# Kernel tuning notes

Hardware: AMD Instinct MI355X
Metric: run time of the kernel (lower is better)

Reference implementation:

```python
import jax, jax.numpy as jnp
import numpy as np

DIM = 1024
NUM_HEADS = 16
HEAD_DIM = DIM // NUM_HEADS


def setup_inputs() -> dict:
    key = jax.random.key(0)
    ks = jax.random.split(key, 9)
    s = 1.0 / np.sqrt(DIM)
    x = jax.random.normal(ks[0], (2, 2048, DIM), dtype=jnp.float32)
    Wq = jax.random.normal(ks[1], (DIM, DIM), dtype=jnp.float32) * s
    bq = jax.random.normal(ks[2], (DIM,), dtype=jnp.float32) * s
    Wk = jax.random.normal(ks[3], (DIM, DIM), dtype=jnp.float32) * s
    bk = jax.random.normal(ks[4], (DIM,), dtype=jnp.float32) * s
    Wv = jax.random.normal(ks[5], (DIM, DIM), dtype=jnp.float32) * s
    bv = jax.random.normal(ks[6], (DIM,), dtype=jnp.float32) * s
    Wo = jax.random.normal(ks[7], (DIM, DIM), dtype=jnp.float32) * s
    bo = jax.random.normal(ks[8], (DIM,), dtype=jnp.float32) * s
    return {"x": x, "Wq": Wq, "bq": bq, "Wk": Wk, "bk": bk,
            "Wv": Wv, "bv": bv, "Wo": Wo, "bo": bo}


def _softmax_one(x, axis=-1):
    # softmax with +1 in the denominator (quiet attention)
    x = x - jnp.max(x, axis=axis, keepdims=True)
    ex = jnp.exp(x)
    return ex / (1.0 + jnp.sum(ex, axis=axis, keepdims=True))


def reference(x, Wq, bq, Wk, bk, Wv, bv, Wo, bo):
    B, L, D = x.shape
    H, hd = NUM_HEADS, HEAD_DIM
    q = (x @ Wq + bq).reshape(B, L, H, hd).transpose(0, 2, 1, 3)  # b h l d
    k = (x @ Wk + bk).reshape(B, L, H, hd).transpose(0, 2, 1, 3)
    v = (x @ Wv + bv).reshape(B, L, H, hd).transpose(0, 2, 1, 3)
    scores = jnp.einsum('bhqd,bhkd->bhqk', q, k) / np.sqrt(hd).astype(np.float32)
    # causal additive mask: -inf above the diagonal (matches torch generate_square_subsequent_mask)
    causal = jnp.triu(jnp.full((L, L), -jnp.inf, dtype=scores.dtype), k=1)
    scores = scores + causal
    attn = _softmax_one(scores, axis=-1)
    ctx = jnp.einsum('bhqk,bhkd->bhqd', attn, v)
    ctx = ctx.transpose(0, 2, 1, 3).reshape(B, L, D)
    return ctx @ Wo + bo
```

## Files before the change

kernel.cpp:

```cpp
#include <hip/hip_runtime.h>
#include <hip/hip_bf16.h>
#include <cstdint>
#include <cstddef>

#define DIMN 1024
#define NHEAD 16
#define HDIM 64
#define NB 2
#define SEQ 2048
#define MROWS 4096
#define BHN 32
#define QKV_STRIDE 4194304
#define BH_ELEMS 131072

typedef float f32x4 __attribute__((ext_vector_type(4)));
typedef __bf16 bf16x8 __attribute__((ext_vector_type(8)));

__device__ __forceinline__ void async_copy16(const void* g, void* l) {
    __builtin_amdgcn_global_load_lds(
        (__attribute__((address_space(1))) void*)(g),
        (__attribute__((address_space(3))) void*)(l), 16, 0, 0);
}

__device__ __forceinline__ unsigned short bf16_bits(float f) {
    __hip_bfloat16 hb = __float2bfloat16(f);
    return *(unsigned short*)&hb;
}

__global__ __launch_bounds__(256) void prep_kernel(
        const float* __restrict__ x, const float* __restrict__ bq,
        const float* __restrict__ bk, const float* __restrict__ bv,
        const float* __restrict__ Wq, const float* __restrict__ Wk,
        const float* __restrict__ Wv, const float* __restrict__ Wo,
        __hip_bfloat16* __restrict__ xbf, float* __restrict__ biasq,
        __hip_bfloat16* __restrict__ wqkvt, __hip_bfloat16* __restrict__ wot) {
    __shared__ float tile[32][33];
    const int bid = blockIdx.x;
    const int t = threadIdx.x;
    if (bid < 4096) {
        int i = (bid * 256 + t) * 4;
        float4 v = *(const float4*)(x + i);
        xbf[i + 0] = __float2bfloat16(v.x);
        xbf[i + 1] = __float2bfloat16(v.y);
        xbf[i + 2] = __float2bfloat16(v.z);
        xbf[i + 3] = __float2bfloat16(v.w);
    } else if (bid < 4099) {
        int base = (bid - 4096) * 1024 + t * 4;
#pragma unroll
        for (int e = 0; e < 4; e++) {
            int gi = base + e;
            int which = gi >> 10, off = gi & 1023;
            float v = (which == 0) ? bq[off] : (which == 1) ? bk[off] : bv[off];
            biasq[gi] = v;
        }
    } else {
        int rr = bid - 4099;
        int z = rr >> 10;
        int tid = rr & 1023;
        int n0 = (tid & 31) * 32, k0 = (tid >> 5) * 32;
        const float* in = (z == 0) ? Wq : (z == 1) ? Wk : (z == 2) ? Wv : Wo;
        __hip_bfloat16* out = (z == 3) ? wot : wqkvt + (size_t)z * DIMN * DIMN;
        int tx = t & 31, ty = t >> 5;
#pragma unroll
        for (int r = 0; r < 32; r += 8)
            tile[ty + r][tx] = in[(size_t)(k0 + ty + r) * DIMN + n0 + tx];
        __syncthreads();
#pragma unroll
        for (int r = 0; r < 32; r += 8)
            out[(size_t)(n0 + ty + r) * DIMN + k0 + tx] =
                __float2bfloat16(tile[tx][ty + r]);
    }
}

__global__ __launch_bounds__(256) void gemm_qkv_kernel(
        const __hip_bfloat16* __restrict__ A, const __hip_bfloat16* __restrict__ Bt,
        const float* __restrict__ bias, __hip_bfloat16* __restrict__ qkv,
        __hip_bfloat16* __restrict__ vt) {
    __shared__ __align__(16) unsigned short As[128 * 32];
    __shared__ __align__(16) unsigned short Bs[128 * 32];
    const int t = threadIdx.x;
    const int m0 = blockIdx.y * 128;
    const int n0 = blockIdx.x * 128;
    const int lane = t & 63;
    const int w = t >> 6;
    const int wm = (w >> 1) * 64;
    const int wn = (w & 1) * 64;
    const int r16 = lane & 15;
    const int quad = lane >> 4;

    f32x4 acc[4][4];
#pragma unroll
    for (int i = 0; i < 4; i++)
#pragma unroll
        for (int j = 0; j < 4; j++) acc[i][j] = (f32x4){0.f, 0.f, 0.f, 0.f};

    const int rowA = t >> 2;
    const int kch = (t & 3) * 8;

    for (int k0 = 0; k0 < DIMN; k0 += 32) {
        __syncthreads();
#pragma unroll
        for (int r = 0; r < 2; r++) {
            int row = rowA + r * 64;
            async_copy16(A + (size_t)(m0 + row) * DIMN + k0 + kch,
                         (char*)As + (size_t)(row * 4 + (t & 3)) * 16);
            async_copy16(Bt + (size_t)(n0 + row) * DIMN + k0 + kch,
                         (char*)Bs + (size_t)(row * 4 + (t & 3)) * 16);
        }
        __syncthreads();

        bf16x8 af[4], bfr[4];
#pragma unroll
        for (int i = 0; i < 4; i++)
            af[i] = *(const bf16x8*)&As[(wm + i * 16 + r16) * 32 + quad * 8];
#pragma unroll
        for (int j = 0; j < 4; j++)
            bfr[j] = *(const bf16x8*)&Bs[(wn + j * 16 + r16) * 32 + quad * 8];
#pragma unroll
        for (int i = 0; i < 4; i++)
#pragma unroll
            for (int j = 0; j < 4; j++)
                acc[i][j] = __builtin_amdgcn_mfma_f32_16x16x32_bf16(
                    af[i], bfr[j], acc[i][j], 0, 0, 0);
    }

#pragma unroll
    for (int i = 0; i < 4; i++)
#pragma unroll
        for (int j = 0; j < 4; j++) {
            int n = n0 + wn + j * 16 + r16;
            float bv = bias[n];
            int which = n >> 10, rem = n & 1023;
            int h = rem >> 6, d = rem & 63;
            int mbase = m0 + wm + i * 16 + quad * 4;
            int b = mbase >> 11;
            int lrow = mbase & 2047;
            int bh = b * NHEAD + h;
            if (which == 2) {
                ushort4 pk;
                pk.x = bf16_bits(acc[i][j][0] + bv);
                pk.y = bf16_bits(acc[i][j][1] + bv);
                pk.z = bf16_bits(acc[i][j][2] + bv);
                pk.w = bf16_bits(acc[i][j][3] + bv);
                *(ushort4*)(vt + (size_t)bh * BH_ELEMS + (size_t)d * SEQ + lrow) = pk;
            } else {
#pragma unroll
                for (int r = 0; r < 4; r++) {
                    float v = acc[i][j][r] + bv;
                    if (which == 0) v *= 0.125f;
                    qkv[(size_t)which * QKV_STRIDE + (size_t)bh * BH_ELEMS +
                        (size_t)(lrow + r) * 64 + d] = __float2bfloat16(v);
                }
            }
        }
}

__global__ __launch_bounds__(256) void gemm_out_kernel(
        const __hip_bfloat16* __restrict__ A, const __hip_bfloat16* __restrict__ Bt,
        const float* __restrict__ bias, float* __restrict__ outp) {
    __shared__ __align__(16) unsigned short As[64 * 32];
    __shared__ __align__(16) unsigned short Bs[128 * 32];
    const int t = threadIdx.x;
    const int m0 = blockIdx.y * 64;
    const int n0 = blockIdx.x * 128;
    const int lane = t & 63;
    const int w = t >> 6;
    const int wm = (w >> 1) * 32;
    const int wn = (w & 1) * 64;
    const int r16 = lane & 15;
    const int quad = lane >> 4;

    f32x4 acc[2][4];
#pragma unroll
    for (int i = 0; i < 2; i++)
#pragma unroll
        for (int j = 0; j < 4; j++) acc[i][j] = (f32x4){0.f, 0.f, 0.f, 0.f};

    const int rowA = t >> 2;
    const int kch = (t & 3) * 8;

    for (int k0 = 0; k0 < DIMN; k0 += 32) {
        __syncthreads();
        async_copy16(A + (size_t)(m0 + rowA) * DIMN + k0 + kch, (char*)As + t * 16);
#pragma unroll
        for (int r = 0; r < 2; r++) {
            int row = rowA + r * 64;
            async_copy16(Bt + (size_t)(n0 + row) * DIMN + k0 + kch,
                         (char*)Bs + (size_t)(row * 4 + (t & 3)) * 16);
        }
        __syncthreads();

        bf16x8 af[2], bfr[4];
#pragma unroll
        for (int i = 0; i < 2; i++)
            af[i] = *(const bf16x8*)&As[(wm + i * 16 + r16) * 32 + quad * 8];
#pragma unroll
        for (int j = 0; j < 4; j++)
            bfr[j] = *(const bf16x8*)&Bs[(wn + j * 16 + r16) * 32 + quad * 8];
#pragma unroll
        for (int i = 0; i < 2; i++)
#pragma unroll
            for (int j = 0; j < 4; j++)
                acc[i][j] = __builtin_amdgcn_mfma_f32_16x16x32_bf16(
                    af[i], bfr[j], acc[i][j], 0, 0, 0);
    }

#pragma unroll
    for (int i = 0; i < 2; i++)
#pragma unroll
        for (int j = 0; j < 4; j++) {
            int n = n0 + wn + j * 16 + r16;
            float bv = bias[n];
#pragma unroll
            for (int r = 0; r < 4; r++) {
                int m = m0 + wm + i * 16 + quad * 4 + r;
                outp[(size_t)m * DIMN + n] = acc[i][j][r] + bv;
            }
        }
}

__global__ __launch_bounds__(512, 4) void attn_mfma_kernel(
        const __hip_bfloat16* __restrict__ qkv, const __hip_bfloat16* __restrict__ vt,
        __hip_bfloat16* __restrict__ ctxout) {
    __shared__ __align__(16) unsigned short SMEM[28672];

    const int bx = blockIdx.x;
    const int g = bx >> 5;
    const int qt = (g < 8) ? 15 - g : g - 8;
    const int bh = bx & 31;
    const int t = threadIdx.x;
    const int lane = t & 63;
    const int w = t >> 6;
    const int half = w >> 2;
    const int wq = w & 3;
    const int r16 = lane & 15;
    const int quad = lane >> 4;
    const int qbase = qt * 128 + wq * 32;
    const int swz = quad ^ ((r16 >> 1) & 3);
    const int pkey = (r16 >> 1) & 3;

    const __hip_bfloat16* Qg = qkv + (size_t)bh * BH_ELEMS;
    const __hip_bfloat16* Kg = qkv + (size_t)QKV_STRIDE + (size_t)bh * BH_ELEMS;
    const __hip_bfloat16* Vtg = vt + (size_t)bh * BH_ELEMS;

    unsigned short* PsW = SMEM + 24576 + w * 512;

    const int cb_kp = (t & 511) >> 8;
    const int cb_rr = ((t & 511) >> 2) & 63;
    const int cb_cg = ((t & 511) & 3) ^ ((cb_rr >> 1) & 3);

    bf16x8 bq[2][2];
#pragma unroll
    for (int ng = 0; ng < 2; ng++)
#pragma unroll
        for (int kp = 0; kp < 2; kp++)
            bq[ng][kp] = *(const bf16x8*)(Qg + (size_t)(qbase + ng * 16 + r16) * 64 +
                                          kp * 32 + quad * 8);

    f32x4 oT[4][2];
#pragma unroll
    for (int mt = 0; mt < 4; mt++)
#pragma unroll
        for (int ng = 0; ng < 2; ng++) oT[mt][ng] = (f32x4){0.f, 0.f, 0.f, 0.f};
    float m_run[2] = {-1e30f, -1e30f};
    float z_run[2] = {0.f, 0.f};

    const int niter = qt + 1;

#pragma unroll
    for (int it = 0; it < 2; it++) {
        int cl = it * 512 + t;
        int ktile = (cl >> 9) ? (qt + 1) : 0;
        async_copy16(Kg + (size_t)(ktile * 64 + cb_rr) * 64 + cb_kp * 32 + cb_cg * 8,
                     (char*)SMEM + (size_t)cl * 16);
    }

#pragma unroll 1
    for (int i = 0; i < niter; i++) {
        const int curb = i & 1;
        __syncthreads();

#pragma unroll
        for (int it = 0; it < 2; it++) {
            int cl = it * 512 + t;
            int ktile = (cl >> 9) ? (qt + 1 + i) : i;
            async_copy16(Vtg + (size_t)cb_rr * SEQ + ktile * 64 + cb_kp * 32 + cb_cg * 8,
                         (char*)SMEM + 32768 + (size_t)cl * 16);
        }
        if (i + 1 < niter) {
            int ktA = i + 1;
            int ktB = qt + 2 + i; if (ktB > 31) ktB = 31;
#pragma unroll
            for (int it = 0; it < 2; it++) {
                int cl = it * 512 + t;
                int ktile = (cl >> 9) ? ktB : ktA;
                async_copy16(Kg + (size_t)(ktile * 64 + cb_rr) * 64 + cb_kp * 32 + cb_cg * 8,
                             (char*)SMEM + (size_t)(curb ^ 1) * 16384 + (size_t)cl * 16);
            }
        }

        const int ktile = half ? (qt + 1 + i) : i;
        const bool active = (ktile * 64 <= qbase + 31);

        f32x4 st[4][2];
        if (active) {
            const unsigned short* KsW = SMEM + curb * 8192 + half * 4096;
#pragma unroll
            for (int mt = 0; mt < 4; mt++)
#pragma unroll
                for (int ng = 0; ng < 2; ng++) st[mt][ng] = (f32x4){0.f, 0.f, 0.f, 0.f};
#pragma unroll
            for (int mt = 0; mt < 4; mt++)
#pragma unroll
                for (int kp = 0; kp < 2; kp++) {
                    bf16x8 ak = *(const bf16x8*)&KsW[kp * 2048 + (mt * 16 + r16) * 32 + swz * 8];
                    st[mt][0] = __builtin_amdgcn_mfma_f32_16x16x32_bf16(ak, bq[0][kp], st[mt][0], 0, 0, 0);
                    st[mt][1] = __builtin_amdgcn_mfma_f32_16x16x32_bf16(ak, bq[1][kp], st[mt][1], 0, 0, 0);
                }

            if (ktile * 64 + 63 > qbase) {
#pragma unroll
                for (int mt = 0; mt < 4; mt++) {
                    int kb = ktile * 64 + mt * 16 + quad * 4;
#pragma unroll
                    for (int ng = 0; ng < 2; ng++) {
                        int q = qbase + ng * 16 + r16;
#pragma unroll
                        for (int r = 0; r < 4; r++)
                            if (kb + r > q) st[mt][ng][r] = -__builtin_inff();
                    }
                }
            }

#pragma unroll
            for (int mt = 0; mt < 4; mt++)
#pragma unroll
                for (int ng = 0; ng < 2; ng++) {
                    float s0 = st[mt][ng][0], s1 = st[mt][ng][1];
                    float s2 = st[mt][ng][2], s3 = st[mt][ng][3];
                    m_run[ng] = fmaxf(m_run[ng], fmaxf(fmaxf(s0, s1), fmaxf(s2, s3)));
                    float p0 = __expf(s0), p1 = __expf(s1);
                    float p2 = __expf(s2), p3 = __expf(s3);
                    z_run[ng] += (p0 + p1) + (p2 + p3);
                    st[mt][ng][0] = p0; st[mt][ng][1] = p1;
                    st[mt][ng][2] = p2; st[mt][ng][3] = p3;
                }
        }
        __syncthreads();

        if (active) {
            const unsigned short* VsW = SMEM + 16384 + half * 4096;
#pragma unroll
            for (int p = 0; p < 2; p++) {
#pragma unroll
                for (int ng = 0; ng < 2; ng++) {
#pragma unroll
                    for (int ml = 0; ml < 2; ml++) {
                        int mt = p * 2 + ml;
                        ushort4 pk;
                        pk.x = bf16_bits(st[mt][ng][0]);
                        pk.y = bf16_bits(st[mt][ng][1]);
                        pk.z = bf16_bits(st[mt][ng][2]);
                        pk.w = bf16_bits(st[mt][ng][3]);
                        int c = (ml * 2 + (quad >> 1)) ^ pkey;
                        *(ushort4*)&PsW[r16 * 32 + c * 8 + (quad & 1) * 4] = pk;
                    }
                    bf16x8 bp = *(const bf16x8*)&PsW[r16 * 32 + (quad ^ pkey) * 8];
#pragma unroll
                    for (int mt = 0; mt < 4; mt++) {
                        bf16x8 av = *(const bf16x8*)&VsW[p * 2048 + (mt * 16 + r16) * 32 + swz * 8];
                        oT[mt][ng] = __builtin_amdgcn_mfma_f32_16x16x32_bf16(
                            av, bp, oT[mt][ng], 0, 0, 0);
                    }
                }
            }
        }
    }

#pragma unroll
    for (int off = 16; off < 64; off <<= 1)
#pragma unroll
        for (int ng = 0; ng < 2; ng++) {
            m_run[ng] = fmaxf(m_run[ng], __shfl_xor(m_run[ng], off, 64));
            z_run[ng] += __shfl_xor(z_run[ng], off, 64);
        }

    __syncthreads();
    f32x4* CbO = (f32x4*)SMEM;
    f32x4* Ml = (f32x4*)((char*)SMEM + 32768);
    if (w >= 4) {
        int w4 = w - 4;
#pragma unroll
        for (int mt = 0; mt < 4; mt++)
#pragma unroll
            for (int ng = 0; ng < 2; ng++)
                CbO[((w4 * 8 + mt * 2 + ng) << 6) + lane] = oT[mt][ng];
        f32x4 ml;
        ml[0] = m_run[0]; ml[1] = m_run[1]; ml[2] = z_run[0]; ml[3] = z_run[1];
        Ml[(w4 << 6) + lane] = ml;
    }
    __syncthreads();
    if (w < 4) {
        f32x4 ml = Ml[(w << 6) + lane];
        float rd[2];
#pragma unroll
        for (int ng = 0; ng < 2; ng++) {
            float mtot = fmaxf(m_run[ng], ml[ng]);
            float ztot = z_run[ng] + ml[2 + ng];
            rd[ng] = 1.f / (__expf(mtot) + ztot);
        }
        const int b = bh >> 4, h = bh & 15;
#pragma unroll
        for (int mt = 0; mt < 4; mt++)
#pragma unroll
            for (int ng = 0; ng < 2; ng++) {
                f32x4 O1 = CbO[((w * 8 + mt * 2 + ng) << 6) + lane];
                int q = qbase + ng * 16 + r16;
                ushort4 pk;
                pk.x = bf16_bits((oT[mt][ng][0] + O1[0]) * rd[ng]);
                pk.y = bf16_bits((oT[mt][ng][1] + O1[1]) * rd[ng]);
                pk.z = bf16_bits((oT[mt][ng][2] + O1[2]) * rd[ng]);
                pk.w = bf16_bits((oT[mt][ng][3] + O1[3]) * rd[ng]);
                *(ushort4*)(ctxout + ((size_t)(b * SEQ + q)) * DIMN + h * 64 +
                            mt * 16 + quad * 4) = pk;
            }
    }
}


extern "C" void kernel_launch(void* const* d_in, const int* in_sizes, int n_in,
                              void* d_out, int out_size, void* d_ws, size_t ws_size,
                              hipStream_t stream) {
    const float* x  = (const float*)d_in[0];
    const float* Wq = (const float*)d_in[1];
    const float* bq = (const float*)d_in[2];
    const float* Wk = (const float*)d_in[3];
    const float* bk = (const float*)d_in[4];
    const float* Wv = (const float*)d_in[5];
    const float* bv = (const float*)d_in[6];
    const float* Wo = (const float*)d_in[7];
    const float* bo = (const float*)d_in[8];

    char* ws = (char*)d_ws;
    __hip_bfloat16* xbf   = (__hip_bfloat16*)(ws);
    __hip_bfloat16* wqkvt = (__hip_bfloat16*)(ws + (8u << 20));
    __hip_bfloat16* wot   = (__hip_bfloat16*)(ws + (14u << 20));
    float*          biasq = (float*)(ws + (16u << 20));
    __hip_bfloat16* qkv   = (__hip_bfloat16*)(ws + (16u << 20) + 65536u);
    __hip_bfloat16* vt    = (__hip_bfloat16*)(ws + (16u << 20) + 65536u + (16u << 20));
    __hip_bfloat16* ctx   = (__hip_bfloat16*)(ws + (16u << 20) + 65536u + (24u << 20));
    float* out = (float*)d_out;

    prep_kernel<<<8195, 256, 0, stream>>>(x, bq, bk, bv, Wq, Wk, Wv, Wo,
                                          xbf, biasq, wqkvt, wot);
    gemm_qkv_kernel<<<dim3(24, 32), 256, 0, stream>>>(xbf, wqkvt, biasq, qkv, vt);
    attn_mfma_kernel<<<512, 512, 0, stream>>>(qkv, vt, ctx);
    gemm_out_kernel<<<dim3(8, 64), 256, 0, stream>>>(ctx, wot, bo, out);
}
```

Before: 178.2 us.

## Stage QKV GEMM epilogue through LDS and single-buffer K in attention

The QKV GEMM now writes its Q and K tiles into a padded shared-memory buffer first. It then stores them to global memory as contiguous 16-byte row segments, replacing the scattered 2-byte stores. The attention kernel drops the K double buffer and loads the next K tile after the score phase, overlapping it with the P·V step instead. That cuts shared memory per block and lets the launch bounds ask for higher occupancy, at the cost of less overlap for K loads and possible register pressure.

New measurement: 407.3 us. 2.29x slower.

```diff
diff --git a/kernel.cpp b/kernel.cpp
--- a/kernel.cpp
+++ b/kernel.cpp
@@ -76,8 +76,9 @@
         const __hip_bfloat16* __restrict__ A, const __hip_bfloat16* __restrict__ Bt,
         const float* __restrict__ bias, __hip_bfloat16* __restrict__ qkv,
         __hip_bfloat16* __restrict__ vt) {
-    __shared__ __align__(16) unsigned short As[128 * 32];
-    __shared__ __align__(16) unsigned short Bs[128 * 32];
+    __shared__ __align__(16) unsigned short SB[128 * 136];
+    unsigned short* As = SB;
+    unsigned short* Bs = SB + 4096;
     const int t = threadIdx.x;
     const int m0 = blockIdx.y * 128;
     const int n0 = blockIdx.x * 128;
@@ -124,35 +125,55 @@
                     af[i], bfr[j], acc[i][j], 0, 0, 0);
     }
 
-#pragma unroll
-    for (int i = 0; i < 4; i++)
-#pragma unroll
-        for (int j = 0; j < 4; j++) {
-            int n = n0 + wn + j * 16 + r16;
-            float bv = bias[n];
-            int which = n >> 10, rem = n & 1023;
-            int h = rem >> 6, d = rem & 63;
-            int mbase = m0 + wm + i * 16 + quad * 4;
-            int b = mbase >> 11;
-            int lrow = mbase & 2047;
-            int bh = b * NHEAD + h;
-            if (which == 2) {
+    const int which = n0 >> 10;
+    if (which == 2) {
+#pragma unroll
+        for (int i = 0; i < 4; i++)
+#pragma unroll
+            for (int j = 0; j < 4; j++) {
+                int n = n0 + wn + j * 16 + r16;
+                float bv = bias[n];
+                int rem = n & 1023;
+                int h = rem >> 6, d = rem & 63;
+                int mbase = m0 + wm + i * 16 + quad * 4;
+                int b = mbase >> 11;
+                int lrow = mbase & 2047;
+                int bh = b * NHEAD + h;
                 ushort4 pk;
                 pk.x = bf16_bits(acc[i][j][0] + bv);
                 pk.y = bf16_bits(acc[i][j][1] + bv);
                 pk.z = bf16_bits(acc[i][j][2] + bv);
                 pk.w = bf16_bits(acc[i][j][3] + bv);
                 *(ushort4*)(vt + (size_t)bh * BH_ELEMS + (size_t)d * SEQ + lrow) = pk;
-            } else {
+            }
+    } else {
+        __syncthreads();
+#pragma unroll
+        for (int i = 0; i < 4; i++)
+#pragma unroll
+            for (int j = 0; j < 4; j++) {
+                int col = wn + j * 16 + r16;
+                float bv = bias[n0 + col];
 #pragma unroll
                 for (int r = 0; r < 4; r++) {
+                    int row = wm + i * 16 + quad * 4 + r;
                     float v = acc[i][j][r] + bv;
                     if (which == 0) v *= 0.125f;
-                    qkv[(size_t)which * QKV_STRIDE + (size_t)bh * BH_ELEMS +
-                        (size_t)(lrow + r) * 64 + d] = __float2bfloat16(v);
+                    SB[row * 136 + col] = bf16_bits(v);
                 }
             }
-        }
+        __syncthreads();
+        int row = t >> 1, seg = t & 1;
+        int m = m0 + row;
+        int b = m >> 11, lrow = m & 2047;
+        int h = ((n0 & 1023) >> 6) + seg;
+        __hip_bfloat16* dst = qkv + (size_t)which * QKV_STRIDE +
+                              (size_t)(b * NHEAD + h) * BH_ELEMS + (size_t)lrow * 64;
+        const unsigned short* src = &SB[row * 136 + seg * 64];
+#pragma unroll
+        for (int c = 0; c < 8; c++)
+            *(uint4*)(dst + c * 8) = *(const uint4*)(src + c * 8);
+    }
 }
 
 __global__ __launch_bounds__(256) void gemm_out_kernel(
@@ -219,10 +240,10 @@
         }
 }
 
-__global__ __launch_bounds__(512, 4) void attn_mfma_kernel(
+__global__ __launch_bounds__(512, 8) void attn_mfma_kernel(
         const __hip_bfloat16* __restrict__ qkv, const __hip_bfloat16* __restrict__ vt,
         __hip_bfloat16* __restrict__ ctxout) {
-    __shared__ __align__(16) unsigned short SMEM[28672];
+    __shared__ __align__(16) unsigned short SMEM[20480];
 
     const int bx = blockIdx.x;
     const int g = bx >> 5;
@@ -243,7 +264,7 @@
     const __hip_bfloat16* Kg = qkv + (size_t)QKV_STRIDE + (size_t)bh * BH_ELEMS;
     const __hip_bfloat16* Vtg = vt + (size_t)bh * BH_ELEMS;
 
-    unsigned short* PsW = SMEM + 24576 + w * 512;
+    unsigned short* PsW = SMEM + 16384 + w * 512;
 
     const int cb_kp = (t & 511) >> 8;
     const int cb_rr = ((t & 511) >> 2) & 63;
@@ -277,7 +298,6 @@
 
 #pragma unroll 1
     for (int i = 0; i < niter; i++) {
-        const int curb = i & 1;
         __syncthreads();
 
 #pragma unroll
@@ -285,18 +305,7 @@
             int cl = it * 512 + t;
             int ktile = (cl >> 9) ? (qt + 1 + i) : i;
             async_copy16(Vtg + (size_t)cb_rr * SEQ + ktile * 64 + cb_kp * 32 + cb_cg * 8,
-                         (char*)SMEM + 32768 + (size_t)cl * 16);
-        }
-        if (i + 1 < niter) {
-            int ktA = i + 1;
-            int ktB = qt + 2 + i; if (ktB > 31) ktB = 31;
-#pragma unroll
-            for (int it = 0; it < 2; it++) {
-                int cl = it * 512 + t;
-                int ktile = (cl >> 9) ? ktB : ktA;
-                async_copy16(Kg + (size_t)(ktile * 64 + cb_rr) * 64 + cb_kp * 32 + cb_cg * 8,
-                             (char*)SMEM + (size_t)(curb ^ 1) * 16384 + (size_t)cl * 16);
-            }
+                         (char*)SMEM + 16384 + (size_t)cl * 16);
         }
 
         const int ktile = half ? (qt + 1 + i) : i;
@@ -304,7 +313,7 @@
 
         f32x4 st[4][2];
         if (active) {
-            const unsigned short* KsW = SMEM + curb * 8192 + half * 4096;
+            const unsigned short* KsW = SMEM + half * 4096;
 #pragma unroll
             for (int mt = 0; mt < 4; mt++)
 #pragma unroll
@@ -348,8 +357,18 @@
         }
         __syncthreads();
 
+        if (i + 1 < niter) {
+#pragma unroll
+            for (int it = 0; it < 2; it++) {
+                int cl = it * 512 + t;
+                int ktile = (cl >> 9) ? (qt + 2 + i) : (i + 1);
+                async_copy16(Kg + (size_t)(ktile * 64 + cb_rr) * 64 + cb_kp * 32 + cb_cg * 8,
+                             (char*)SMEM + (size_t)cl * 16);
+            }
+        }
+
         if (active) {
-            const unsigned short* VsW = SMEM + 16384 + half * 4096;
+            const unsigned short* VsW = SMEM + 8192 + half * 4096;
 #pragma unroll
             for (int p = 0; p < 2; p++) {
 #pragma unroll
```
